# Kernel optimization log

Measured on AMD Instinct MI355X. Metric: run time of the kernel, lower is better.

The kernel has to match this reference:

```python
import jax, jax.numpy as jnp
import numpy as np

N_EMBED = 1024
N_HEADS = 16
HEAD = N_EMBED // N_HEADS
EPS = 1e-5


def setup_inputs() -> dict:
    key = jax.random.key(0)
    ks = jax.random.split(key, 16)
    C = N_EMBED
    s = lambda fan_in: 1.0 / np.sqrt(fan_in)
    return {
        "x": jax.random.normal(ks[0], (4, 2048, C), jnp.float32),
        "ln1_g": jnp.ones((C,), jnp.float32),
        "ln1_b": jnp.zeros((C,), jnp.float32),
        "w_attn": jax.random.normal(ks[1], (C, 3 * C), jnp.float32) * s(C),
        "b_attn": jnp.zeros((3 * C,), jnp.float32),
        "w_proj": jax.random.normal(ks[2], (C, C), jnp.float32) * s(C),
        "b_proj": jnp.zeros((C,), jnp.float32),
        "ln2_g": jnp.ones((C,), jnp.float32),
        "ln2_b": jnp.zeros((C,), jnp.float32),
        "w_fc": jax.random.normal(ks[3], (C, 4 * C), jnp.float32) * s(C),
        "b_fc": jnp.zeros((4 * C,), jnp.float32),
        "w_fc2": jax.random.normal(ks[4], (4 * C, C), jnp.float32) * s(4 * C),
        "b_fc2": jnp.zeros((C,), jnp.float32),
    }


def _layernorm(x, g, b):
    mu = jnp.mean(x, axis=-1, keepdims=True)
    var = jnp.mean(jnp.square(x - mu), axis=-1, keepdims=True)
    return (x - mu) * jax.lax.rsqrt(var + EPS) * g + b


def _attention(x, w_attn, b_attn, w_proj, b_proj):
    B, T, C = x.shape
    qkv = x @ w_attn + b_attn  # [B,T,3C]
    q, k, v = jnp.split(qkv, 3, axis=-1)
    q = q.reshape(B, T, N_HEADS, HEAD).transpose(0, 2, 1, 3)  # [B,H,T,D]
    k = k.reshape(B, T, N_HEADS, HEAD).transpose(0, 2, 1, 3)
    v = v.reshape(B, T, N_HEADS, HEAD).transpose(0, 2, 1, 3)
    scale = 1.0 / np.sqrt(HEAD)
    affin = jnp.einsum("bhqd,bhkd->bhqk", q, k) * scale  # [B,H,T,T]
    causal = jnp.tril(jnp.ones((T, T), bool))
    affin = jnp.where(causal, affin, -jnp.inf)
    affin = jax.nn.softmax(affin, axis=-1)
    y = jnp.einsum("bhqk,bhkd->bhqd", affin, v)  # [B,H,T,D]
    y = y.transpose(0, 2, 1, 3).reshape(B, T, C)
    return y @ w_proj + b_proj


def reference(x, ln1_g, ln1_b, w_attn, b_attn, w_proj, b_proj,
              ln2_g, ln2_b, w_fc, b_fc, w_fc2, b_fc2):
    x = x + _attention(_layernorm(x, ln1_g, ln1_b), w_attn, b_attn, w_proj, b_proj)
    h = _layernorm(x, ln2_g, ln2_b)
    h = jax.nn.gelu(h @ w_fc + b_fc, approximate=True)  # tanh GELU
    x = x + (h @ w_fc2 + b_fc2)
    return x
```

## Files before the change

kernel.cpp:

```cpp
#include <hip/hip_runtime.h>
#include <math.h>


#define M_ROWS 8192
#define T_SEQ 2048
#define N_EMB 1024
#define N_HEADS 16
#define HEAD_D 64

typedef _Float16 f16;
typedef __attribute__((ext_vector_type(8))) _Float16 f16x8;
typedef __attribute__((ext_vector_type(4))) _Float16 f16x4;
typedef __attribute__((ext_vector_type(4))) float f32x4;

__device__ __forceinline__ void async16(void* lds, const void* g) {
    __builtin_amdgcn_global_load_lds(
        (const __attribute__((address_space(1))) unsigned int*)g,
        (__attribute__((address_space(3))) unsigned int*)lds, 16, 0, 0);
}

__device__ __forceinline__ float gelu_tanh(float v) {
    float u = 0.7978845608028654f * (v + 0.044715f * v * v * v);
    float e = __expf(2.0f * u);
    float t = 1.0f - 2.0f / (e + 1.0f);
    return 0.5f * v * (1.0f + t);
}

__launch_bounds__(256)
__global__ void wconv_kernel(const float* __restrict__ W, f16* __restrict__ WT,
                             int K, int N) {
    __shared__ float t[32][33];
    int tx = threadIdx.x & 31, ty = threadIdx.x >> 5;
    int n0 = blockIdx.x * 32, k0 = blockIdx.y * 32;
    #pragma unroll
    for (int r = 0; r < 4; r++)
        t[ty * 4 + r][tx] = W[(size_t)(k0 + ty * 4 + r) * N + n0 + tx];
    __syncthreads();
    #pragma unroll
    for (int r = 0; r < 4; r++)
        WT[(size_t)(n0 + ty * 4 + r) * K + k0 + tx] = (f16)t[tx][ty * 4 + r];
}

__launch_bounds__(256)
__global__ void ln_kernel(const float* __restrict__ x, const float* __restrict__ g,
                          const float* __restrict__ b, f16* __restrict__ y) {
    int row = blockIdx.x;
    int tid = threadIdx.x;
    const float* xr = x + (size_t)row * N_EMB;
    float4 v = *(const float4*)(xr + tid * 4);
    float s  = v.x + v.y + v.z + v.w;
    float sq = v.x * v.x + v.y * v.y + v.z * v.z + v.w * v.w;
    #pragma unroll
    for (int off = 32; off > 0; off >>= 1) {
        s  += __shfl_down(s, off);
        sq += __shfl_down(sq, off);
    }
    __shared__ float ws_[4], wq_[4];
    __shared__ float mean_s, rstd_s;
    int lane = tid & 63, wid = tid >> 6;
    if (lane == 0) { ws_[wid] = s; wq_[wid] = sq; }
    __syncthreads();
    if (tid == 0) {
        float st = ws_[0] + ws_[1] + ws_[2] + ws_[3];
        float qt = wq_[0] + wq_[1] + wq_[2] + wq_[3];
        float mu = st * (1.0f / N_EMB);
        float var = qt * (1.0f / N_EMB) - mu * mu;
        mean_s = mu;
        rstd_s = rsqrtf(var + 1e-5f);
    }
    __syncthreads();
    float mu = mean_s, r = rstd_s;
    float4 gv = *(const float4*)(g + tid * 4);
    float4 bv = *(const float4*)(b + tid * 4);
    f16x4 o;
    o.x = (f16)((v.x - mu) * r * gv.x + bv.x);
    o.y = (f16)((v.y - mu) * r * gv.y + bv.y);
    o.z = (f16)((v.z - mu) * r * gv.z + bv.z);
    o.w = (f16)((v.w - mu) * r * gv.w + bv.w);
    *(f16x4*)(y + (size_t)row * N_EMB + tid * 4) = o;
}

template <int EPI, int BM, int BN>
__launch_bounds__(512, 2)
__global__ void gemm8(const f16* __restrict__ A, const f16* __restrict__ Bt,
                      const float* __restrict__ bias, const float* __restrict__ res,
                      float* __restrict__ Cf, f16* __restrict__ Ch,
                      f16* __restrict__ vT, int K, int N) {
    constexpr int MI = BM / 32;
    constexpr int MH = MI / 2;
    constexpr int NJ = BN / 64;
    constexpr int AROUNDS = BM / 64;
    constexpr int BROUNDS = BN / 64;
    constexpr int ROUNDS = AROUNDS + BROUNDS;
    constexpr int P1E = (ROUNDS == 8) ? 3 : 2;
    constexpr int P2E = (ROUNDS == 8) ? 6 : 4;
    __shared__ f16 As[2][BM * 64];
    __shared__ f16 Bs[2][BN * 64];

    int tid = threadIdx.x;
    int lane = tid & 63, wave = tid >> 6;
    int wr = wave >> 2, wc = wave & 3;
    int quad = lane >> 4, l16 = lane & 15;

    int nx = gridDim.x, nwg = nx * gridDim.y;
    int orig = blockIdx.y * nx + blockIdx.x;
    int cpx = nwg >> 3;
    int swz = (orig & 7) * cpx + (orig >> 3);
    int m0 = (swz / nx) * BM, n0 = (swz % nx) * BN;

    int srow = tid >> 3;
    int sglog = (tid & 7) ^ (srow & 7);
    const f16* pa[AROUNDS];
    const f16* pb[BROUNDS];
    #pragma unroll
    for (int r = 0; r < AROUNDS; r++)
        pa[r] = A + (size_t)(m0 + r * 64 + srow) * K + sglog * 8;
    #pragma unroll
    for (int r = 0; r < BROUNDS; r++)
        pb[r] = Bt + (size_t)(n0 + r * 64 + srow) * K + sglog * 8;

    int nt = K >> 6;

    auto stage = [&](int t, int buf, int r) {
        if (r < AROUNDS)
            async16((char*)As[buf] + (size_t)(r * 512 + tid) * 16,
                    pa[r] + (size_t)t * 64);
        else
            async16((char*)Bs[buf] + (size_t)((r - AROUNDS) * 512 + tid) * 16,
                    pb[r - AROUNDS] + (size_t)t * 64);
    };

    #pragma unroll
    for (int r = 0; r < ROUNDS; r++) stage(0, 0, r);

    f32x4 acc[MI][NJ] = {};
    for (int t = 0; t < nt; t++) {
        int p = t & 1;
        asm volatile("s_waitcnt vmcnt(0)" ::: "memory");
        __builtin_amdgcn_s_barrier();
        const f16* as = As[p];
        const f16* bs = Bs[p];
        bool pf = (t + 1 < nt);
        f16x8 a0[MH], a1[MH], b0[NJ], b1[NJ];

        if (pf) {
            #pragma unroll
            for (int r = 0; r < P1E; r++) stage(t + 1, p ^ 1, r);
        }
        #pragma unroll
        for (int i = 0; i < MH; i++) {
            int row = wr * (BM / 2) + i * 16 + l16;
            a0[i] = *(const f16x8*)&as[row * 64 + ((quad) ^ (row & 7)) * 8];
        }
        #pragma unroll
        for (int j = 0; j < NJ; j++) {
            int row = wc * (BN / 4) + j * 16 + l16;
            b0[j] = *(const f16x8*)&bs[row * 64 + ((quad) ^ (row & 7)) * 8];
        }
        asm volatile("s_waitcnt lgkmcnt(0)" ::: "memory");
        __builtin_amdgcn_s_setprio(1);
        #pragma unroll
        for (int i = 0; i < MH; i++) {
            #pragma unroll
            for (int j = 0; j < NJ; j++)
                acc[i][j] = __builtin_amdgcn_mfma_f32_16x16x32_f16(
                    a0[i], b0[j], acc[i][j], 0, 0, 0);
        }
        __builtin_amdgcn_s_setprio(0);
        __builtin_amdgcn_s_barrier();

        if (pf) {
            #pragma unroll
            for (int r = P1E; r < P2E; r++) stage(t + 1, p ^ 1, r);
        }
        #pragma unroll
        for (int i = 0; i < MH; i++) {
            int row = wr * (BM / 2) + (MH + i) * 16 + l16;
            a1[i] = *(const f16x8*)&as[row * 64 + ((quad) ^ (row & 7)) * 8];
        }
        asm volatile("s_waitcnt lgkmcnt(0)" ::: "memory");
        __builtin_amdgcn_s_setprio(1);
        #pragma unroll
        for (int i = 0; i < MH; i++) {
            #pragma unroll
            for (int j = 0; j < NJ; j++)
                acc[MH + i][j] = __builtin_amdgcn_mfma_f32_16x16x32_f16(
                    a1[i], b0[j], acc[MH + i][j], 0, 0, 0);
        }
        __builtin_amdgcn_s_setprio(0);
        __builtin_amdgcn_s_barrier();

        if (pf) {
            #pragma unroll
            for (int r = P2E; r < ROUNDS; r++) stage(t + 1, p ^ 1, r);
        }
        #pragma unroll
        for (int i = 0; i < MH; i++) {
            int row = wr * (BM / 2) + i * 16 + l16;
            a0[i] = *(const f16x8*)&as[row * 64 + ((4 + quad) ^ (row & 7)) * 8];
        }
        #pragma unroll
        for (int j = 0; j < NJ; j++) {
            int row = wc * (BN / 4) + j * 16 + l16;
            b1[j] = *(const f16x8*)&bs[row * 64 + ((4 + quad) ^ (row & 7)) * 8];
        }
        asm volatile("s_waitcnt lgkmcnt(0)" ::: "memory");
        __builtin_amdgcn_s_setprio(1);
        #pragma unroll
        for (int i = 0; i < MH; i++) {
            #pragma unroll
            for (int j = 0; j < NJ; j++)
                acc[i][j] = __builtin_amdgcn_mfma_f32_16x16x32_f16(
                    a0[i], b1[j], acc[i][j], 0, 0, 0);
        }
        __builtin_amdgcn_s_setprio(0);
        __builtin_amdgcn_s_barrier();

        #pragma unroll
        for (int i = 0; i < MH; i++) {
            int row = wr * (BM / 2) + (MH + i) * 16 + l16;
            a1[i] = *(const f16x8*)&as[row * 64 + ((4 + quad) ^ (row & 7)) * 8];
        }
        asm volatile("s_waitcnt lgkmcnt(0)" ::: "memory");
        __builtin_amdgcn_s_setprio(1);
        #pragma unroll
        for (int i = 0; i < MH; i++) {
            #pragma unroll
            for (int j = 0; j < NJ; j++)
                acc[MH + i][j] = __builtin_amdgcn_mfma_f32_16x16x32_f16(
                    a1[i], b1[j], acc[MH + i][j], 0, 0, 0);
        }
        __builtin_amdgcn_s_setprio(0);
        __builtin_amdgcn_s_barrier();
    }

    #pragma unroll
    for (int i = 0; i < MI; i++) {
        int row0 = m0 + wr * (BM / 2) + i * 16 + quad * 4;
        #pragma unroll
        for (int j = 0; j < NJ; j++) {
            int col = n0 + wc * (BN / 4) + j * 16 + l16;
            float bb = bias[col];
            if (EPI == 3) {
                if (n0 < 2048) {
                    #pragma unroll
                    for (int r = 0; r < 4; r++)
                        Ch[(size_t)(row0 + r) * 2048 + col] = (f16)(acc[i][j][r] + bb);
                } else {
                    int hh = (col - 2048) >> 6, dd = col & 63;
                    int bb_ = row0 >> 11, t0 = row0 & 2047;
                    f16x4 pk;
                    pk.x = (f16)(acc[i][j][0] + bb);
                    pk.y = (f16)(acc[i][j][1] + bb);
                    pk.z = (f16)(acc[i][j][2] + bb);
                    pk.w = (f16)(acc[i][j][3] + bb);
                    *(f16x4*)(vT + ((size_t)(bb_ * 16 + hh) * 64 + dd) * 2048 + t0) = pk;
                }
            } else {
                #pragma unroll
                for (int r = 0; r < 4; r++) {
                    size_t idx = (size_t)(row0 + r) * N + col;
                    float v = acc[i][j][r] + bb;
                    if (EPI == 1) v += res[idx];
                    if (EPI == 2) Ch[idx] = (f16)gelu_tanh(v);
                    else          Cf[idx] = v;
                }
            }
        }
    }
}

__launch_bounds__(256, 2)
__global__ void flash_kernel(const f16* __restrict__ qk, const f16* __restrict__ vT,
                             f16* __restrict__ y) {
    __shared__ __align__(16) char smem[67584];
    f16* Ks = (f16*)smem;
    f16* Vs = (f16*)(smem + 16384);
    int tid = threadIdx.x;
    int lane = tid & 63, w = tid >> 6;
    int quad = lane >> 4, l16 = lane & 15;
    f16* Ps = (f16*)(smem + 32768 + w * 8704);

    int bh = blockIdx.y;
    int b = bh >> 4, h = bh & 15;

    for (int half = 0; half < 2; half++) {
        int qt = half ? (int)blockIdx.x : 15 - (int)blockIdx.x;
        int q0 = qt * 128;

        f16x8 qf[2][2];
        #pragma unroll
        for (int qn = 0; qn < 2; qn++) {
            int q = q0 + w * 32 + qn * 16 + l16;
            #pragma unroll
            for (int dblk = 0; dblk < 2; dblk++) {
                f16x8 t = *(const f16x8*)(qk + (size_t)(b * T_SEQ + q) * 2048 +
                                          h * 64 + dblk * 32 + quad * 8);
                #pragma unroll
                for (int e = 0; e < 8; e++) t[e] = t[e] * (f16)0.125f;
                qf[qn][dblk] = t;
            }
        }

        float m_r[2] = {-INFINITY, -INFINITY};
        float l_r[2] = {0.0f, 0.0f};
        f32x4 Oacc[2][4] = {};

        for (int jt = 0; jt <= qt; jt++) {
            int j0 = jt * 128;
            __syncthreads();
            #pragma unroll
            for (int i = 0; i < 4; i++) {
                int L = i * 256 + tid;
                int j = L >> 3, g1 = L & 7;
                int g = g1 ^ (j & 7);
                async16((char*)Ks + (size_t)L * 16,
                        qk + (size_t)(b * T_SEQ + j0 + j) * 2048 + 1024 + h * 64 + g * 8);
            }
            #pragma unroll
            for (int i = 0; i < 4; i++) {
                int L = i * 256 + tid;
                int d = L >> 4, g1 = L & 15;
                int g = (g1 & 8) | ((g1 ^ d) & 7);
                async16((char*)Vs + (size_t)L * 16,
                        vT + ((size_t)(bh) * 64 + d) * 2048 + j0 + g * 8);
            }
            __syncthreads();

            f32x4 S[8][2];
            #pragma unroll
            for (int jm = 0; jm < 8; jm++) {
                f16x8 kf[2];
                #pragma unroll
                for (int dblk = 0; dblk < 2; dblk++) {
                    int j = jm * 16 + l16;
                    int g = (dblk * 4 + quad) ^ (j & 7);
                    kf[dblk] = *(const f16x8*)(Ks + (size_t)(j * 8 + g) * 8);
                }
                #pragma unroll
                for (int qn = 0; qn < 2; qn++) {
                    f32x4 s = {};
                    s = __builtin_amdgcn_mfma_f32_16x16x32_f16(kf[0], qf[qn][0], s, 0, 0, 0);
                    s = __builtin_amdgcn_mfma_f32_16x16x32_f16(kf[1], qf[qn][1], s, 0, 0, 0);
                    S[jm][qn] = s;
                }
            }

            if (jt == qt) {
                #pragma unroll
                for (int jm = 0; jm < 8; jm++)
                    #pragma unroll
                    for (int qn = 0; qn < 2; qn++)
                        #pragma unroll
                        for (int r = 0; r < 4; r++) {
                            int jl = jm * 16 + quad * 4 + r;
                            int ql = w * 32 + qn * 16 + l16;
                            if (jl > ql) S[jm][qn][r] = -1e30f;
                        }
            }

            float alpha[2];
            #pragma unroll
            for (int qn = 0; qn < 2; qn++) {
                float tmax = -INFINITY;
                #pragma unroll
                for (int jm = 0; jm < 8; jm++)
                    #pragma unroll
                    for (int r = 0; r < 4; r++)
                        tmax = fmaxf(tmax, S[jm][qn][r]);
                tmax = fmaxf(tmax, __shfl_xor(tmax, 16));
                tmax = fmaxf(tmax, __shfl_xor(tmax, 32));
                float mnew = fmaxf(m_r[qn], tmax);
                alpha[qn] = __expf(m_r[qn] - mnew);
                m_r[qn] = mnew;
                float rsum = 0.0f;
                #pragma unroll
                for (int jm = 0; jm < 8; jm++)
                    #pragma unroll
                    for (int r = 0; r < 4; r++) {
                        float p = __expf(S[jm][qn][r] - mnew);
                        S[jm][qn][r] = p;
                        rsum += p;
                    }
                rsum += __shfl_xor(rsum, 16);
                rsum += __shfl_xor(rsum, 32);
                l_r[qn] = l_r[qn] * alpha[qn] + rsum;
            }

            #pragma unroll
            for (int jm = 0; jm < 8; jm++)
                #pragma unroll
                for (int qn = 0; qn < 2; qn++) {
                    f16x4 pk;
                    pk.x = (f16)S[jm][qn][0];
                    pk.y = (f16)S[jm][qn][1];
                    pk.z = (f16)S[jm][qn][2];
                    pk.w = (f16)S[jm][qn][3];
                    *(f16x4*)(Ps + (size_t)(qn * 16 + l16) * 136 + jm * 16 + quad * 4) = pk;
                }

            float aPV[2][4];
            #pragma unroll
            for (int m = 0; m < 2; m++)
                #pragma unroll
                for (int r = 0; r < 4; r++)
                    aPV[m][r] = __shfl(alpha[m], quad * 20 + r);
            #pragma unroll
            for (int m = 0; m < 2; m++)
                #pragma unroll
                for (int n = 0; n < 4; n++)
                    #pragma unroll
                    for (int r = 0; r < 4; r++)
                        Oacc[m][n][r] *= aPV[m][r];

            #pragma unroll
            for (int kblk = 0; kblk < 4; kblk++) {
                f16x8 pf[2];
                #pragma unroll
                for (int m = 0; m < 2; m++)
                    pf[m] = *(const f16x8*)(Ps + (size_t)(m * 16 + l16) * 136 +
                                            kblk * 32 + quad * 8);
                f16x8 vf[4];
                #pragma unroll
                for (int n = 0; n < 4; n++) {
                    int d = n * 16 + l16;
                    int g = (kblk * 4 + quad);
                    int gs = (g & 8) | ((g ^ d) & 7);
                    vf[n] = *(const f16x8*)(Vs + (size_t)(d * 16 + gs) * 8);
                }
                #pragma unroll
                for (int m = 0; m < 2; m++)
                    #pragma unroll
                    for (int n = 0; n < 4; n++)
                        Oacc[m][n] = __builtin_amdgcn_mfma_f32_16x16x32_f16(
                            pf[m], vf[n], Oacc[m][n], 0, 0, 0);
            }
        }

        #pragma unroll
        for (int m = 0; m < 2; m++) {
            float lPV[4];
            #pragma unroll
            for (int r = 0; r < 4; r++)
                lPV[r] = 1.0f / __shfl(l_r[m], quad * 20 + r);
            #pragma unroll
            for (int n = 0; n < 4; n++) {
                #pragma unroll
                for (int r = 0; r < 4; r++) {
                    int q = q0 + w * 32 + m * 16 + quad * 4 + r;
                    y[(size_t)(b * T_SEQ + q) * N_EMB + h * 64 + n * 16 + l16] =
                        (f16)(Oacc[m][n][r] * lPV[r]);
                }
            }
        }
    }
}

extern "C" void kernel_launch(void* const* d_in, const int* in_sizes, int n_in,
                              void* d_out, int out_size, void* d_ws, size_t ws_size,
                              hipStream_t stream) {
    const float* x      = (const float*)d_in[0];
    const float* ln1_g  = (const float*)d_in[1];
    const float* ln1_b  = (const float*)d_in[2];
    const float* w_attn = (const float*)d_in[3];
    const float* b_attn = (const float*)d_in[4];
    const float* w_proj = (const float*)d_in[5];
    const float* b_proj = (const float*)d_in[6];
    const float* ln2_g  = (const float*)d_in[7];
    const float* ln2_b  = (const float*)d_in[8];
    const float* w_fc   = (const float*)d_in[9];
    const float* b_fc   = (const float*)d_in[10];
    const float* w_fc2  = (const float*)d_in[11];
    const float* b_fc2  = (const float*)d_in[12];
    float* out = (float*)d_out;

    const size_t MB = 1024 * 1024;
    char* ws = (char*)d_ws;
    f16*   lnbuf = (f16*)ws;
    f16*   qkbuf = (f16*)(ws + 16 * MB);
    f16*   vTbuf = (f16*)(ws + 48 * MB);
    f16*   ybuf  = (f16*)(ws + 64 * MB);
    f16*   h     = (f16*)(ws + 80 * MB);
    f16*   wT    = (f16*)(ws + 144 * MB);
    f16* wT_attn = wT;
    f16* wT_proj = wT_attn + (size_t)3072 * 1024;
    f16* wT_fc   = wT_proj + (size_t)1024 * 1024;
    f16* wT_fc2  = wT_fc   + (size_t)1024 * 4096;

    wconv_kernel<<<dim3(3072 / 32, 1024 / 32), 256, 0, stream>>>(w_attn, wT_attn, 1024, 3072);
    wconv_kernel<<<dim3(1024 / 32, 1024 / 32), 256, 0, stream>>>(w_proj, wT_proj, 1024, 1024);
    wconv_kernel<<<dim3(4096 / 32, 1024 / 32), 256, 0, stream>>>(w_fc,   wT_fc,   1024, 4096);
    wconv_kernel<<<dim3(1024 / 32, 4096 / 32), 256, 0, stream>>>(w_fc2,  wT_fc2,  4096, 1024);

    ln_kernel<<<M_ROWS, 256, 0, stream>>>(x, ln1_g, ln1_b, lnbuf);
    gemm8<3, 256, 256><<<dim3(3072 / 256, M_ROWS / 256), 512, 0, stream>>>(
        lnbuf, wT_attn, b_attn, nullptr, nullptr, qkbuf, vTbuf, 1024, 3072);
    flash_kernel<<<dim3(8, 64), 256, 0, stream>>>(qkbuf, vTbuf, ybuf);
    gemm8<1, 128, 256><<<dim3(1024 / 256, M_ROWS / 128), 512, 0, stream>>>(
        ybuf, wT_proj, b_proj, x, out, nullptr, nullptr, 1024, 1024);
    ln_kernel<<<M_ROWS, 256, 0, stream>>>(out, ln2_g, ln2_b, lnbuf);
    gemm8<2, 256, 256><<<dim3(4096 / 256, M_ROWS / 256), 512, 0, stream>>>(
        lnbuf, wT_fc, b_fc, nullptr, nullptr, h, nullptr, 1024, 4096);
    gemm8<1, 128, 256><<<dim3(1024 / 256, M_ROWS / 128), 512, 0, stream>>>(
        h, wT_fc2, b_fc2, out, out, nullptr, nullptr, 4096, 1024);
}
```

Before: 587.2 us.

## Add smaller-tile high-occupancy GEMM for QKV and FC, restructure residual GEMM pipeline

Adds a new gemmX kernel for the QKV and FC1 GEMMs. It uses 128x256 tiles with a K-step of 32, a single MFMA phase per step, and launch bounds allowing 4 workgroups per CU. The residual GEMM (gemm8) is reworked to issue the next tile's prefetch before waiting, with a partial vmcnt wait and a two-phase inner loop over full MI. The aim is higher occupancy and better overlap of global-to-LDS loads with MFMA. The cost is less data reuse per tile and more barriers per unit of K.

```diff
diff --git a/kernel.cpp b/kernel.cpp
--- a/kernel.cpp
+++ b/kernel.cpp
@@ -80,23 +80,14 @@
     *(f16x4*)(y + (size_t)row * N_EMB + tid * 4) = o;
 }
 
-template <int EPI, int BM, int BN>
-__launch_bounds__(512, 2)
-__global__ void gemm8(const f16* __restrict__ A, const f16* __restrict__ Bt,
-                      const float* __restrict__ bias, const float* __restrict__ res,
+template <int EPI>
+__launch_bounds__(512, 4)
+__global__ void gemmX(const f16* __restrict__ A, const f16* __restrict__ Bt,
+                      const float* __restrict__ bias,
                       float* __restrict__ Cf, f16* __restrict__ Ch,
                       f16* __restrict__ vT, int K, int N) {
-    constexpr int MI = BM / 32;
-    constexpr int MH = MI / 2;
-    constexpr int NJ = BN / 64;
-    constexpr int AROUNDS = BM / 64;
-    constexpr int BROUNDS = BN / 64;
-    constexpr int ROUNDS = AROUNDS + BROUNDS;
-    constexpr int P1E = (ROUNDS == 8) ? 3 : 2;
-    constexpr int P2E = (ROUNDS == 8) ? 6 : 4;
-    __shared__ f16 As[2][BM * 64];
-    __shared__ f16 Bs[2][BN * 64];
-
+    __shared__ f16 As[2][128 * 32];
+    __shared__ f16 Bs[2][256 * 32];
     int tid = threadIdx.x;
     int lane = tid & 63, wave = tid >> 6;
     int wr = wave >> 2, wc = wave & 3;
@@ -106,140 +97,70 @@
     int orig = blockIdx.y * nx + blockIdx.x;
     int cpx = nwg >> 3;
     int swz = (orig & 7) * cpx + (orig >> 3);
-    int m0 = (swz / nx) * BM, n0 = (swz % nx) * BN;
-
-    int srow = tid >> 3;
-    int sglog = (tid & 7) ^ (srow & 7);
-    const f16* pa[AROUNDS];
-    const f16* pb[BROUNDS];
-    #pragma unroll
-    for (int r = 0; r < AROUNDS; r++)
-        pa[r] = A + (size_t)(m0 + r * 64 + srow) * K + sglog * 8;
-    #pragma unroll
-    for (int r = 0; r < BROUNDS; r++)
-        pb[r] = Bt + (size_t)(n0 + r * 64 + srow) * K + sglog * 8;
-
-    int nt = K >> 6;
-
-    auto stage = [&](int t, int buf, int r) {
-        if (r < AROUNDS)
-            async16((char*)As[buf] + (size_t)(r * 512 + tid) * 16,
-                    pa[r] + (size_t)t * 64);
-        else
-            async16((char*)Bs[buf] + (size_t)((r - AROUNDS) * 512 + tid) * 16,
-                    pb[r - AROUNDS] + (size_t)t * 64);
+    int m0 = (swz / nx) * 128, n0 = (swz % nx) * 256;
+
+    int srow = tid >> 2;
+    int sg = (tid & 3) ^ ((srow >> 1) & 3);
+    const f16* pA  = A  + (size_t)(m0 + srow) * K + sg * 8;
+    const f16* pB0 = Bt + (size_t)(n0 + srow) * K + sg * 8;
+    const f16* pB1 = Bt + (size_t)(n0 + 128 + srow) * K + sg * 8;
+    char* dA  = (char*)As + (size_t)tid * 16;
+    char* dB0 = (char*)Bs + (size_t)tid * 16;
+    char* dB1 = (char*)Bs + (size_t)(512 + tid) * 16;
+
+    int nt = K >> 5;
+
+    auto stage = [&](int t, int buf) {
+        async16(dA  + buf * 8192,  pA  + (size_t)t * 32);
+        async16(dB0 + buf * 16384, pB0 + (size_t)t * 32);
+        async16(dB1 + buf * 16384, pB1 + (size_t)t * 32);
     };
 
-    #pragma unroll
-    for (int r = 0; r < ROUNDS; r++) stage(0, 0, r);
-
-    f32x4 acc[MI][NJ] = {};
+    stage(0, 0);
+
+    f32x4 acc[4][4] = {};
     for (int t = 0; t < nt; t++) {
         int p = t & 1;
-        asm volatile("s_waitcnt vmcnt(0)" ::: "memory");
-        __builtin_amdgcn_s_barrier();
+        if (t + 1 < nt) {
+            stage(t + 1, p ^ 1);
+            asm volatile("s_waitcnt vmcnt(3)" ::: "memory");
+        } else {
+            asm volatile("s_waitcnt vmcnt(0)" ::: "memory");
+        }
+        __builtin_amdgcn_s_barrier();
+
         const f16* as = As[p];
         const f16* bs = Bs[p];
-        bool pf = (t + 1 < nt);
-        f16x8 a0[MH], a1[MH], b0[NJ], b1[NJ];
-
-        if (pf) {
-            #pragma unroll
-            for (int r = 0; r < P1E; r++) stage(t + 1, p ^ 1, r);
-        }
-        #pragma unroll
-        for (int i = 0; i < MH; i++) {
-            int row = wr * (BM / 2) + i * 16 + l16;
-            a0[i] = *(const f16x8*)&as[row * 64 + ((quad) ^ (row & 7)) * 8];
-        }
-        #pragma unroll
-        for (int j = 0; j < NJ; j++) {
-            int row = wc * (BN / 4) + j * 16 + l16;
-            b0[j] = *(const f16x8*)&bs[row * 64 + ((quad) ^ (row & 7)) * 8];
+        f16x8 av[4], bv[4];
+        #pragma unroll
+        for (int i = 0; i < 4; i++) {
+            int row = wr * 64 + i * 16 + l16;
+            av[i] = *(const f16x8*)&as[row * 32 + (quad ^ ((row >> 1) & 3)) * 8];
+        }
+        #pragma unroll
+        for (int j = 0; j < 4; j++) {
+            int row = wc * 64 + j * 16 + l16;
+            bv[j] = *(const f16x8*)&bs[row * 32 + (quad ^ ((row >> 1) & 3)) * 8];
         }
         asm volatile("s_waitcnt lgkmcnt(0)" ::: "memory");
         __builtin_amdgcn_s_setprio(1);
         #pragma unroll
-        for (int i = 0; i < MH; i++) {
-            #pragma unroll
-            for (int j = 0; j < NJ; j++)
+        for (int i = 0; i < 4; i++) {
+            #pragma unroll
+            for (int j = 0; j < 4; j++)
                 acc[i][j] = __builtin_amdgcn_mfma_f32_16x16x32_f16(
-                    a0[i], b0[j], acc[i][j], 0, 0, 0);
+                    av[i], bv[j], acc[i][j], 0, 0, 0);
         }
         __builtin_amdgcn_s_setprio(0);
         __builtin_amdgcn_s_barrier();
-
-        if (pf) {
-            #pragma unroll
-            for (int r = P1E; r < P2E; r++) stage(t + 1, p ^ 1, r);
-        }
-        #pragma unroll
-        for (int i = 0; i < MH; i++) {
-            int row = wr * (BM / 2) + (MH + i) * 16 + l16;
-            a1[i] = *(const f16x8*)&as[row * 64 + ((quad) ^ (row & 7)) * 8];
-        }
-        asm volatile("s_waitcnt lgkmcnt(0)" ::: "memory");
-        __builtin_amdgcn_s_setprio(1);
-        #pragma unroll
-        for (int i = 0; i < MH; i++) {
-            #pragma unroll
-            for (int j = 0; j < NJ; j++)
-                acc[MH + i][j] = __builtin_amdgcn_mfma_f32_16x16x32_f16(
-                    a1[i], b0[j], acc[MH + i][j], 0, 0, 0);
-        }
-        __builtin_amdgcn_s_setprio(0);
-        __builtin_amdgcn_s_barrier();
-
-        if (pf) {
-            #pragma unroll
-            for (int r = P2E; r < ROUNDS; r++) stage(t + 1, p ^ 1, r);
-        }
-        #pragma unroll
-        for (int i = 0; i < MH; i++) {
-            int row = wr * (BM / 2) + i * 16 + l16;
-            a0[i] = *(const f16x8*)&as[row * 64 + ((4 + quad) ^ (row & 7)) * 8];
-        }
-        #pragma unroll
-        for (int j = 0; j < NJ; j++) {
-            int row = wc * (BN / 4) + j * 16 + l16;
-            b1[j] = *(const f16x8*)&bs[row * 64 + ((4 + quad) ^ (row & 7)) * 8];
-        }
-        asm volatile("s_waitcnt lgkmcnt(0)" ::: "memory");
-        __builtin_amdgcn_s_setprio(1);
-        #pragma unroll
-        for (int i = 0; i < MH; i++) {
-            #pragma unroll
-            for (int j = 0; j < NJ; j++)
-                acc[i][j] = __builtin_amdgcn_mfma_f32_16x16x32_f16(
-                    a0[i], b1[j], acc[i][j], 0, 0, 0);
-        }
-        __builtin_amdgcn_s_setprio(0);
-        __builtin_amdgcn_s_barrier();
-
-        #pragma unroll
-        for (int i = 0; i < MH; i++) {
-            int row = wr * (BM / 2) + (MH + i) * 16 + l16;
-            a1[i] = *(const f16x8*)&as[row * 64 + ((4 + quad) ^ (row & 7)) * 8];
-        }
-        asm volatile("s_waitcnt lgkmcnt(0)" ::: "memory");
-        __builtin_amdgcn_s_setprio(1);
-        #pragma unroll
-        for (int i = 0; i < MH; i++) {
-            #pragma unroll
-            for (int j = 0; j < NJ; j++)
-                acc[MH + i][j] = __builtin_amdgcn_mfma_f32_16x16x32_f16(
-                    a1[i], b1[j], acc[MH + i][j], 0, 0, 0);
-        }
-        __builtin_amdgcn_s_setprio(0);
-        __builtin_amdgcn_s_barrier();
-    }
-
-    #pragma unroll
-    for (int i = 0; i < MI; i++) {
-        int row0 = m0 + wr * (BM / 2) + i * 16 + quad * 4;
-        #pragma unroll
-        for (int j = 0; j < NJ; j++) {
-            int col = n0 + wc * (BN / 4) + j * 16 + l16;
+    }
+
+    #pragma unroll
+    for (int i = 0; i < 4; i++) {
+        int row0 = m0 + wr * 64 + i * 16 + quad * 4;
+        #pragma unroll
+        for (int j = 0; j < 4; j++) {
+            int col = n0 + wc * 64 + j * 16 + l16;
             float bb = bias[col];
             if (EPI == 3) {
                 if (n0 < 2048) {
@@ -260,11 +181,143 @@
                 #pragma unroll
                 for (int r = 0; r < 4; r++) {
                     size_t idx = (size_t)(row0 + r) * N + col;
-                    float v = acc[i][j][r] + bb;
-                    if (EPI == 1) v += res[idx];
-                    if (EPI == 2) Ch[idx] = (f16)gelu_tanh(v);
-                    else          Cf[idx] = v;
-                }
+                    Ch[idx] = (f16)gelu_tanh(acc[i][j][r] + bb);
+                }
+            }
+        }
+    }
+}
+
+template <int EPI, int BM, int BN>
+__launch_bounds__(512, 2)
+__global__ void gemm8(const f16* __restrict__ A, const f16* __restrict__ Bt,
+                      const float* __restrict__ bias, const float* __restrict__ res,
+                      float* __restrict__ Cf, int K, int N) {
+    constexpr int MI = BM / 32;
+    constexpr int NJ = BN / 64;
+    constexpr int AROUNDS = BM / 64;
+    constexpr int BROUNDS = BN / 64;
+    constexpr int ROUNDS = AROUNDS + BROUNDS;
+    constexpr int P1E = 3;
+    __shared__ f16 As[2][BM * 64];
+    __shared__ f16 Bs[2][BN * 64];
+
+    int tid = threadIdx.x;
+    int lane = tid & 63, wave = tid >> 6;
+    int wr = wave >> 2, wc = wave & 3;
+    int quad = lane >> 4, l16 = lane & 15;
+
+    int nx = gridDim.x, nwg = nx * gridDim.y;
+    int orig = blockIdx.y * nx + blockIdx.x;
+    int cpx = nwg >> 3;
+    int swz = (orig & 7) * cpx + (orig >> 3);
+    int m0 = (swz / nx) * BM, n0 = (swz % nx) * BN;
+
+    int srow = tid >> 3;
+    int sglog = (tid & 7) ^ (srow & 7);
+    const f16* pa[AROUNDS];
+    const f16* pb[BROUNDS];
+    #pragma unroll
+    for (int r = 0; r < AROUNDS; r++)
+        pa[r] = A + (size_t)(m0 + r * 64 + srow) * K + sglog * 8;
+    #pragma unroll
+    for (int r = 0; r < BROUNDS; r++)
+        pb[r] = Bt + (size_t)(n0 + r * 64 + srow) * K + sglog * 8;
+
+    int nt = K >> 6;
+
+    auto stage = [&](int t, int buf, int r) {
+        if (r < AROUNDS)
+            async16((char*)As[buf] + (size_t)(r * 512 + tid) * 16,
+                    pa[r] + (size_t)t * 64);
+        else
+            async16((char*)Bs[buf] + (size_t)((r - AROUNDS) * 512 + tid) * 16,
+                    pb[r - AROUNDS] + (size_t)t * 64);
+    };
+
+    #pragma unroll
+    for (int r = 0; r < ROUNDS; r++) stage(0, 0, r);
+
+    f32x4 acc[MI][NJ] = {};
+    for (int t = 0; t < nt; t++) {
+        int p = t & 1;
+        bool pf = (t + 1 < nt);
+
+        if (pf) {
+            #pragma unroll
+            for (int r = 0; r < P1E; r++) stage(t + 1, p ^ 1, r);
+            asm volatile("s_waitcnt vmcnt(3)" ::: "memory");
+        } else {
+            asm volatile("s_waitcnt vmcnt(0)" ::: "memory");
+        }
+        __builtin_amdgcn_s_barrier();
+
+        const f16* as = As[p];
+        const f16* bs = Bs[p];
+        f16x8 av[MI], bv[NJ];
+
+        #pragma unroll
+        for (int i = 0; i < MI; i++) {
+            int row = wr * (BM / 2) + i * 16 + l16;
+            av[i] = *(const f16x8*)&as[row * 64 + ((quad) ^ (row & 7)) * 8];
+        }
+        #pragma unroll
+        for (int j = 0; j < NJ; j++) {
+            int row = wc * (BN / 4) + j * 16 + l16;
+            bv[j] = *(const f16x8*)&bs[row * 64 + ((quad) ^ (row & 7)) * 8];
+        }
+        if (pf) {
+            #pragma unroll
+            for (int r = P1E; r < ROUNDS; r++) stage(t + 1, p ^ 1, r);
+        }
+        __builtin_amdgcn_s_barrier();
+        asm volatile("s_waitcnt lgkmcnt(0)" ::: "memory");
+        __builtin_amdgcn_s_setprio(1);
+        #pragma unroll
+        for (int i = 0; i < MI; i++) {
+            #pragma unroll
+            for (int j = 0; j < NJ; j++)
+                acc[i][j] = __builtin_amdgcn_mfma_f32_16x16x32_f16(
+                    av[i], bv[j], acc[i][j], 0, 0, 0);
+        }
+        __builtin_amdgcn_s_setprio(0);
+        __builtin_amdgcn_s_barrier();
+
+        #pragma unroll
+        for (int i = 0; i < MI; i++) {
+            int row = wr * (BM / 2) + i * 16 + l16;
+            av[i] = *(const f16x8*)&as[row * 64 + ((4 + quad) ^ (row & 7)) * 8];
+        }
+        #pragma unroll
+        for (int j = 0; j < NJ; j++) {
+            int row = wc * (BN / 4) + j * 16 + l16;
+            bv[j] = *(const f16x8*)&bs[row * 64 + ((4 + quad) ^ (row & 7)) * 8];
+        }
+        __builtin_amdgcn_s_barrier();
+        asm volatile("s_waitcnt lgkmcnt(0)" ::: "memory");
+        __builtin_amdgcn_s_setprio(1);
+        #pragma unroll
+        for (int i = 0; i < MI; i++) {
+            #pragma unroll
+            for (int j = 0; j < NJ; j++)
+                acc[i][j] = __builtin_amdgcn_mfma_f32_16x16x32_f16(
+                    av[i], bv[j], acc[i][j], 0, 0, 0);
+        }
+        __builtin_amdgcn_s_setprio(0);
+        __builtin_amdgcn_s_barrier();
+    }
+
+    #pragma unroll
+    for (int i = 0; i < MI; i++) {
+        int row0 = m0 + wr * (BM / 2) + i * 16 + quad * 4;
+        #pragma unroll
+        for (int j = 0; j < NJ; j++) {
+            int col = n0 + wc * (BN / 4) + j * 16 + l16;
+            float bb = bias[col];
+            #pragma unroll
+            for (int r = 0; r < 4; r++) {
+                size_t idx = (size_t)(row0 + r) * N + col;
+                Cf[idx] = acc[i][j][r] + bb + res[idx];
             }
         }
     }
@@ -493,14 +546,14 @@
     wconv_kernel<<<dim3(1024 / 32, 4096 / 32), 256, 0, stream>>>(w_fc2,  wT_fc2,  4096, 1024);
 
     ln_kernel<<<M_ROWS, 256, 0, stream>>>(x, ln1_g, ln1_b, lnbuf);
-    gemm8<3, 256, 256><<<dim3(3072 / 256, M_ROWS / 256), 512, 0, stream>>>(
-        lnbuf, wT_attn, b_attn, nullptr, nullptr, qkbuf, vTbuf, 1024, 3072);
+    gemmX<3><<<dim3(3072 / 256, M_ROWS / 128), 512, 0, stream>>>(
+        lnbuf, wT_attn, b_attn, nullptr, qkbuf, vTbuf, 1024, 3072);
     flash_kernel<<<dim3(8, 64), 256, 0, stream>>>(qkbuf, vTbuf, ybuf);
     gemm8<1, 128, 256><<<dim3(1024 / 256, M_ROWS / 128), 512, 0, stream>>>(
-        ybuf, wT_proj, b_proj, x, out, nullptr, nullptr, 1024, 1024);
+        ybuf, wT_proj, b_proj, x, out, 1024, 1024);
     ln_kernel<<<M_ROWS, 256, 0, stream>>>(out, ln2_g, ln2_b, lnbuf);
-    gemm8<2, 256, 256><<<dim3(4096 / 256, M_ROWS / 256), 512, 0, stream>>>(
-        lnbuf, wT_fc, b_fc, nullptr, nullptr, h, nullptr, 1024, 4096);
+    gemmX<2><<<dim3(4096 / 256, M_ROWS / 128), 512, 0, stream>>>(
+        lnbuf, wT_fc, b_fc, nullptr, h, nullptr, 1024, 4096);
     gemm8<1, 128, 256><<<dim3(1024 / 256, M_ROWS / 128), 512, 0, stream>>>(
-        h, wT_fc2, b_fc2, out, out, nullptr, nullptr, 4096, 1024);
-}
+        h, wT_fc2, b_fc2, out, out, 4096, 1024);
+}
```

Measured after the change: 511.4 us. 1.15x faster.
